# Kernel tuning notes

Hardware: AMD Instinct MI355X
Metric: run time of the kernel (lower is better)

The kernel has to match this reference:

```python
import jax, jax.numpy as jnp
import numpy as np

N = 20000
E = 320000
IN_FEATS = 512
H = 4
D_HID = 256
D_OUT = 256
NEG_SLOPE = 0.2


def _gat_layer(h, src, dst, Wsrc, Wdst, al, ar, b, apply_act):
    # h: [N, Fin]; Wsrc/Wdst: [Fin, H*D]; al/ar: [H, D]; b: [H*D]
    Hh, Dd = al.shape
    fs = (h @ Wsrc).reshape(-1, Hh, Dd)  # [N, H, D] src projection
    fd = (h @ Wdst).reshape(-1, Hh, Dd)  # [N, H, D] dst projection
    el = (fs * al).sum(-1)               # [N, H]
    er = (fd * ar).sum(-1)               # [N, H]
    e = jax.nn.leaky_relu(el[src] + er[dst], NEG_SLOPE)  # [E, H]
    m = jax.lax.stop_gradient(jax.ops.segment_max(e, dst, num_segments=N))
    m = jnp.where(jnp.isfinite(m), m, 0.0)
    ex = jnp.exp(e - m[dst])
    den = jax.ops.segment_sum(ex, dst, num_segments=N)  # [N, H]
    alpha = ex / den[dst]                               # edge softmax per dst node
    msg = fs[src] * alpha[:, :, None]                   # [E, H, D]
    out = jax.ops.segment_sum(msg, dst, num_segments=N) + b.reshape(Hh, Dd)
    if apply_act:
        out = jax.nn.relu(out)
    return out  # [N, H, D]


def setup_inputs() -> dict:
    key = jax.random.key(0)
    ks = jax.random.split(key, 20)
    x = jax.random.normal(ks[0], (N, IN_FEATS), dtype=jnp.float32)
    src = jax.random.randint(ks[1], (E,), 0, N, dtype=jnp.int32)
    dst = jax.random.randint(ks[2], (E,), 0, N, dtype=jnp.int32)
    fins = [IN_FEATS, H * D_HID, H * D_HID]
    douts = [D_HID, D_HID, D_OUT]
    inp = {"x": x, "src": src, "dst": dst}
    ki = 3
    for l in range(3):
        fin, do = fins[l], douts[l]
        s = 1.0 / np.sqrt(fin)
        inp[f"Wsrc{l}"] = jax.random.normal(ks[ki], (fin, H * do), dtype=jnp.float32) * s; ki += 1
        inp[f"Wdst{l}"] = jax.random.normal(ks[ki], (fin, H * do), dtype=jnp.float32) * s; ki += 1
        inp[f"al{l}"] = jax.random.normal(ks[ki], (H, do), dtype=jnp.float32) * 0.1; ki += 1
        inp[f"ar{l}"] = jax.random.normal(ks[ki], (H, do), dtype=jnp.float32) * 0.1; ki += 1
        inp[f"b{l}"] = jnp.zeros((H * do,), dtype=jnp.float32)
    return inp


def reference(x, src, dst,
              Wsrc0, Wdst0, al0, ar0, b0,
              Wsrc1, Wdst1, al1, ar1, b1,
              Wsrc2, Wdst2, al2, ar2, b2):
    h = _gat_layer(x, src, dst, Wsrc0, Wdst0, al0, ar0, b0, True).reshape(N, -1)
    h = _gat_layer(h, src, dst, Wsrc1, Wdst1, al1, ar1, b1, True).reshape(N, -1)
    h = _gat_layer(h, src, dst, Wsrc2, Wdst2, al2, ar2, b2, False)  # [N, H, D_OUT]
    return h.mean(axis=1)  # [N, D_OUT]
```

## Files before the change

kernel.cpp:

```cpp
#include <hip/hip_runtime.h>
#include <hip/hip_bf16.h>
#include <math.h>

#define NNODES 20000
#define NPAD   20480
#define NBM    160
#define NEDGES 320000
#define HEADS  4
#define DDIM   256
#define MCOLS  1024

typedef __attribute__((ext_vector_type(8))) short short8;
typedef __attribute__((ext_vector_type(4))) float f32x4;

__device__ __forceinline__ unsigned short f2bf(float f) {
  unsigned u = __float_as_uint(f);
  unsigned r = (u + 0x7fffu + ((u >> 16) & 1u)) >> 16;
  return (unsigned short)r;
}
__device__ __forceinline__ float bf2f(unsigned short h) {
  return __uint_as_float(((unsigned)h) << 16);
}

__device__ __forceinline__ void async_ld16(void* lds, const void* g) {
  __builtin_amdgcn_global_load_lds(
      (const __attribute__((address_space(1))) unsigned int*)g,
      (__attribute__((address_space(3))) unsigned int*)lds, 16, 0, 0);
}

__global__ void k_zero(int* deg, int n) {
  int i = blockIdx.x*blockDim.x + threadIdx.x;
  if (i < n) deg[i] = 0;
}
__global__ void k_hist(const int* __restrict__ dst, int* deg, int e) {
  int i = blockIdx.x*blockDim.x + threadIdx.x;
  if (i < e) atomicAdd(&deg[dst[i]], 1);
}
__global__ void k_scan(const int* __restrict__ deg, int* row_ptr, int* cursor) {
  __shared__ int sm[1024];
  int t = threadIdx.x;
  const int CH = 20;
  int base = t*CH;
  int s = 0;
  #pragma unroll
  for (int i = 0; i < CH; ++i) { int idx = base+i; if (idx < NNODES) s += deg[idx]; }
  int val = s;
  sm[t] = s; __syncthreads();
  for (int off = 1; off < 1024; off <<= 1) {
    int add = (t >= off) ? sm[t-off] : 0;
    __syncthreads();
    val += add; sm[t] = val;
    __syncthreads();
  }
  int run = val - s;
  for (int i = 0; i < CH; ++i) {
    int idx = base+i;
    if (idx < NNODES) { row_ptr[idx] = run; cursor[idx] = run; run += deg[idx]; }
  }
  if (t == 0) row_ptr[NNODES] = NEDGES;
}
__global__ void k_fill(const int* __restrict__ src, const int* __restrict__ dst,
                       int* cursor, int* srcs_sorted, int* dsts_sorted, int e) {
  int i = blockIdx.x*blockDim.x + threadIdx.x;
  if (i < e) {
    int d = dst[i];
    int pos = atomicAdd(&cursor[d], 1);
    srcs_sorted[pos] = src[i];
    dsts_sorted[pos] = d;
  }
}

__global__ void k_wgt(const float* __restrict__ el, const float* __restrict__ er,
                      const int* __restrict__ srcs, const int* __restrict__ dsts,
                      float* __restrict__ w, int e4) {
  int i = blockIdx.x*blockDim.x + threadIdx.x;
  if (i >= e4) return;
  int pos = i >> 2, h = i & 3;
  float v = el[srcs[pos]*HEADS + h] + er[dsts[pos]*HEADS + h];
  v = v >= 0.f ? v : 0.2f*v;
  w[i] = __expf(v);
}

__global__ void k_fold(const float* __restrict__ W, const float* __restrict__ v,
                       float* __restrict__ F, int K) {
  int wave = threadIdx.x >> 6, lane = threadIdx.x & 63;
  int p = blockIdx.x*4 + wave;
  if (p >= K*HEADS) return;
  int k = p >> 2, h = p & 3;
  const float4 wv = *(const float4*)&W[(size_t)k*MCOLS + h*DDIM + lane*4];
  const float4 av = *(const float4*)&v[h*DDIM + lane*4];
  float s = wv.x*av.x + wv.y*av.y + wv.z*av.z + wv.w*av.w;
  for (int off = 32; off; off >>= 1) s += __shfl_xor(s, off);
  if (lane == 0) F[k*HEADS + h] = s;
}

__global__ void k_cvt_a(const float* __restrict__ x, unsigned short* __restrict__ hi,
                        unsigned short* __restrict__ lo, int total, int total_pad) {
  int i = blockIdx.x*blockDim.x + threadIdx.x;
  int idx = i*4;
  if (idx >= total_pad) return;
  float4 v = (idx < total) ? *(const float4*)&x[idx] : make_float4(0.f,0.f,0.f,0.f);
  ushort4 h, l;
  h.x = f2bf(v.x); l.x = f2bf(v.x - bf2f(h.x));
  h.y = f2bf(v.y); l.y = f2bf(v.y - bf2f(h.y));
  h.z = f2bf(v.z); l.z = f2bf(v.z - bf2f(h.z));
  h.w = f2bf(v.w); l.w = f2bf(v.w - bf2f(h.w));
  *(ushort4*)&hi[idx] = h;
  *(ushort4*)&lo[idx] = l;
}

__global__ __launch_bounds__(256) void k_cvt_w(const float* __restrict__ W,
                                               unsigned short* __restrict__ Th, int K) {
  __shared__ float sm[32][33];
  int k0 = blockIdx.y*32, n0 = blockIdx.x*32;
  int t = threadIdx.x;
  int r = t >> 3, c4 = (t & 7)*4;
  *(float4*)&sm[r][c4] = *(const float4*)&W[(size_t)(k0 + r)*MCOLS + n0 + c4];
  __syncthreads();
  ushort4 h;
  h.x = f2bf(sm[c4+0][r]);
  h.y = f2bf(sm[c4+1][r]);
  h.z = f2bf(sm[c4+2][r]);
  h.w = f2bf(sm[c4+3][r]);
  *(ushort4*)&Th[(size_t)(n0 + r)*K + k0 + c4] = h;
}

__global__ void k_eler0(const float* __restrict__ x, const float* __restrict__ Wal,
                        const float* __restrict__ Wred,
                        float* __restrict__ el, float* __restrict__ er) {
  int n = blockIdx.x;
  int h = threadIdx.x >> 6, lane = threadIdx.x & 63;
  float sl = 0.f, sr = 0.f;
  for (int k = lane; k < 512; k += 64) {
    float xv = x[(size_t)n*512 + k];
    sl = fmaf(xv, Wal[k*HEADS + h], sl);
    sr = fmaf(xv, Wred[k*HEADS + h], sr);
  }
  for (int off = 32; off; off >>= 1) { sl += __shfl_xor(sl, off); sr += __shfl_xor(sr, off); }
  if (lane == 0) { el[n*HEADS + h] = sl; er[n*HEADS + h] = sr; }
}

__global__ __launch_bounds__(256, 3) void k_gemm_mfma(
    const unsigned short* __restrict__ Ah, const unsigned short* __restrict__ Al,
    const unsigned short* __restrict__ Bh,
    unsigned short* __restrict__ Fh, int K) {
  __shared__ short sAh[128*32], sAl[128*32], sBh[128*32];
  const int t = threadIdx.x;
  const int w = t >> 6, l = t & 63;
  const int b = blockIdx.x;
  const int xcd = b & 7, kk = b >> 3;
  const int bm = xcd*20 + (kk >> 3), bn = kk & 7;
  const int m0 = (w >> 1) * 64, n0 = (w & 1) * 64;

  f32x4 acc[4][4];
  #pragma unroll
  for (int i = 0; i < 4; ++i)
    #pragma unroll
    for (int j = 0; j < 4; ++j) acc[i][j] = (f32x4){0.f, 0.f, 0.f, 0.f};

  const int srow = t >> 2, koct = (t & 3) * 8;
  const size_t r64 = (size_t)64 * K;
  const unsigned short* gAh = Ah + (size_t)(bm*128 + srow)*K + koct;
  const unsigned short* gAl = Al + (size_t)(bm*128 + srow)*K + koct;
  const unsigned short* gBh = Bh + (size_t)(bn*128 + srow)*K + koct;
  char* lAh = (char*)sAh + w*1024;
  char* lAl = (char*)sAl + w*1024;
  char* lBh = (char*)sBh + w*1024;

  const int fr = l & 15, fq = l >> 4;

  for (int k0 = 0; k0 < K; k0 += 32) {
    async_ld16(lAh,        gAh + k0);
    async_ld16(lAh + 4096, gAh + k0 + r64);
    async_ld16(lAl,        gAl + k0);
    async_ld16(lAl + 4096, gAl + k0 + r64);
    async_ld16(lBh,        gBh + k0);
    async_ld16(lBh + 4096, gBh + k0 + r64);
    __syncthreads();

    short8 bhv[4];
    #pragma unroll
    for (int nt = 0; nt < 4; ++nt)
      bhv[nt] = *(const short8*)&sBh[(n0 + nt*16 + fr)*32 + fq*8];
    #pragma unroll
    for (int mt = 0; mt < 4; ++mt) {
      int off = (m0 + mt*16 + fr)*32 + fq*8;
      short8 ah = *(const short8*)&sAh[off];
      short8 al = *(const short8*)&sAl[off];
      #pragma unroll
      for (int nt = 0; nt < 4; ++nt) {
        acc[mt][nt] = __builtin_amdgcn_mfma_f32_16x16x32_bf16(ah, bhv[nt], acc[mt][nt], 0, 0, 0);
        acc[mt][nt] = __builtin_amdgcn_mfma_f32_16x16x32_bf16(al, bhv[nt], acc[mt][nt], 0, 0, 0);
      }
    }
    __syncthreads();
  }

  #pragma unroll
  for (int mt = 0; mt < 4; ++mt)
    #pragma unroll
    for (int nt = 0; nt < 4; ++nt) {
      size_t base = (size_t)(bm*128 + m0 + mt*16 + fq*4)*MCOLS + bn*128 + n0 + nt*16 + fr;
      Fh[base          ] = f2bf(acc[mt][nt][0]);
      Fh[base + MCOLS  ] = f2bf(acc[mt][nt][1]);
      Fh[base + 2*MCOLS] = f2bf(acc[mt][nt][2]);
      Fh[base + 3*MCOLS] = f2bf(acc[mt][nt][3]);
    }
}

__global__ __launch_bounds__(256) void k_agg_f(
    const unsigned short* __restrict__ fsh, const float* __restrict__ wbuf,
    const int* __restrict__ row_ptr, const int* __restrict__ srcs,
    const float* __restrict__ bias,
    const float* __restrict__ WalN, const float* __restrict__ WredN,
    unsigned short* __restrict__ Ahi, unsigned short* __restrict__ Alo,
    float* __restrict__ el_next, float* __restrict__ er_next) {
  __shared__ float red_sm[HEADS][8];
  int n = blockIdx.x;
  int h = threadIdx.x >> 6, lane = threadIdx.x & 63;
  int k0 = h*DDIM + lane*4;
  if (n >= NNODES) {
    ushort4 z = {0,0,0,0};
    *(ushort4*)&Ahi[(size_t)n*MCOLS + k0] = z;
    *(ushort4*)&Alo[(size_t)n*MCOLS + k0] = z;
    return;
  }
  int beg = row_ptr[n], end = row_ptr[n+1];
  float den = 0.f;
  float4 acc = make_float4(0.f, 0.f, 0.f, 0.f);
  const char* fbyte = (const char*)fsh;
  const unsigned tb = (unsigned)(k0*2);
  int i = beg;
  for (; i + 3 < end; i += 4) {
    float w0 = wbuf[(size_t)(i  )*HEADS + h];
    float w1 = wbuf[(size_t)(i+1)*HEADS + h];
    float w2 = wbuf[(size_t)(i+2)*HEADS + h];
    float w3 = wbuf[(size_t)(i+3)*HEADS + h];
    unsigned o0 = (unsigned)srcs[i  ]*2048u + tb;
    unsigned o1 = (unsigned)srcs[i+1]*2048u + tb;
    unsigned o2 = (unsigned)srcs[i+2]*2048u + tb;
    unsigned o3 = (unsigned)srcs[i+3]*2048u + tb;
    const ushort4 u0 = *(const ushort4*)(fbyte + o0);
    const ushort4 u1 = *(const ushort4*)(fbyte + o1);
    const ushort4 u2 = *(const ushort4*)(fbyte + o2);
    const ushort4 u3 = *(const ushort4*)(fbyte + o3);
    den += (w0 + w1) + (w2 + w3);
    acc.x = fmaf(w0, bf2f(u0.x), fmaf(w1, bf2f(u1.x), fmaf(w2, bf2f(u2.x), fmaf(w3, bf2f(u3.x), acc.x))));
    acc.y = fmaf(w0, bf2f(u0.y), fmaf(w1, bf2f(u1.y), fmaf(w2, bf2f(u2.y), fmaf(w3, bf2f(u3.y), acc.y))));
    acc.z = fmaf(w0, bf2f(u0.z), fmaf(w1, bf2f(u1.z), fmaf(w2, bf2f(u2.z), fmaf(w3, bf2f(u3.z), acc.z))));
    acc.w = fmaf(w0, bf2f(u0.w), fmaf(w1, bf2f(u1.w), fmaf(w2, bf2f(u2.w), fmaf(w3, bf2f(u3.w), acc.w))));
  }
  for (; i < end; ++i) {
    float wgt = wbuf[(size_t)i*HEADS + h];
    unsigned o = (unsigned)srcs[i]*2048u + tb;
    const ushort4 u = *(const ushort4*)(fbyte + o);
    den += wgt;
    acc.x = fmaf(wgt, bf2f(u.x), acc.x);
    acc.y = fmaf(wgt, bf2f(u.y), acc.y);
    acc.z = fmaf(wgt, bf2f(u.z), acc.z);
    acc.w = fmaf(wgt, bf2f(u.w), acc.w);
  }
  float inv = den > 0.f ? 1.f/den : 0.f;
  const float4 bv = *(const float4*)&bias[k0];
  float4 o;
  o.x = fmaxf(acc.x*inv + bv.x, 0.f);
  o.y = fmaxf(acc.y*inv + bv.y, 0.f);
  o.z = fmaxf(acc.z*inv + bv.z, 0.f);
  o.w = fmaxf(acc.w*inv + bv.w, 0.f);
  ushort4 hv, lv;
  hv.x = f2bf(o.x); lv.x = f2bf(o.x - bf2f(hv.x));
  hv.y = f2bf(o.y); lv.y = f2bf(o.y - bf2f(hv.y));
  hv.z = f2bf(o.z); lv.z = f2bf(o.z - bf2f(hv.z));
  hv.w = f2bf(o.w); lv.w = f2bf(o.w - bf2f(hv.w));
  *(ushort4*)&Ahi[(size_t)n*MCOLS + k0] = hv;
  *(ushort4*)&Alo[(size_t)n*MCOLS + k0] = lv;
  const float4 a0 = *(const float4*)&WalN[(k0+0)*HEADS];
  const float4 a1 = *(const float4*)&WalN[(k0+1)*HEADS];
  const float4 a2 = *(const float4*)&WalN[(k0+2)*HEADS];
  const float4 a3 = *(const float4*)&WalN[(k0+3)*HEADS];
  const float4 q0 = *(const float4*)&WredN[(k0+0)*HEADS];
  const float4 q1 = *(const float4*)&WredN[(k0+1)*HEADS];
  const float4 q2 = *(const float4*)&WredN[(k0+2)*HEADS];
  const float4 q3 = *(const float4*)&WredN[(k0+3)*HEADS];
  float p[8];
  p[0] = o.x*a0.x + o.y*a1.x + o.z*a2.x + o.w*a3.x;
  p[1] = o.x*a0.y + o.y*a1.y + o.z*a2.y + o.w*a3.y;
  p[2] = o.x*a0.z + o.y*a1.z + o.z*a2.z + o.w*a3.z;
  p[3] = o.x*a0.w + o.y*a1.w + o.z*a2.w + o.w*a3.w;
  p[4] = o.x*q0.x + o.y*q1.x + o.z*q2.x + o.w*q3.x;
  p[5] = o.x*q0.y + o.y*q1.y + o.z*q2.y + o.w*q3.y;
  p[6] = o.x*q0.z + o.y*q1.z + o.z*q2.z + o.w*q3.z;
  p[7] = o.x*q0.w + o.y*q1.w + o.z*q2.w + o.w*q3.w;
  for (int off = 32; off; off >>= 1)
    #pragma unroll
    for (int j = 0; j < 8; ++j) p[j] += __shfl_xor(p[j], off);
  if (lane == 0)
    #pragma unroll
    for (int j = 0; j < 8; ++j) red_sm[h][j] = p[j];
  __syncthreads();
  if (threadIdx.x < 8) {
    int t = threadIdx.x;
    float v = (red_sm[0][t] + red_sm[1][t]) + (red_sm[2][t] + red_sm[3][t]);
    if (t < 4) el_next[n*HEADS + t] = v;
    else       er_next[n*HEADS + (t-4)] = v;
  }
}

__global__ __launch_bounds__(256) void k_agg_out(
    const unsigned short* __restrict__ fsh, const float* __restrict__ wbuf,
    const int* __restrict__ row_ptr, const int* __restrict__ srcs,
    const float* __restrict__ bias, float* __restrict__ out) {
  __shared__ float sm[HEADS*DDIM];
  int n = blockIdx.x;
  int h = threadIdx.x >> 6, lane = threadIdx.x & 63;
  int beg = row_ptr[n], end = row_ptr[n+1];
  float den = 0.f;
  float4 acc = make_float4(0.f, 0.f, 0.f, 0.f);
  const char* fbyte = (const char*)fsh;
  const unsigned tb = (unsigned)((h*DDIM + lane*4)*2);
  int i = beg;
  for (; i + 3 < end; i += 4) {
    float w0 = wbuf[(size_t)(i  )*HEADS + h];
    float w1 = wbuf[(size_t)(i+1)*HEADS + h];
    float w2 = wbuf[(size_t)(i+2)*HEADS + h];
    float w3 = wbuf[(size_t)(i+3)*HEADS + h];
    unsigned o0 = (unsigned)srcs[i  ]*2048u + tb;
    unsigned o1 = (unsigned)srcs[i+1]*2048u + tb;
    unsigned o2 = (unsigned)srcs[i+2]*2048u + tb;
    unsigned o3 = (unsigned)srcs[i+3]*2048u + tb;
    const ushort4 u0 = *(const ushort4*)(fbyte + o0);
    const ushort4 u1 = *(const ushort4*)(fbyte + o1);
    const ushort4 u2 = *(const ushort4*)(fbyte + o2);
    const ushort4 u3 = *(const ushort4*)(fbyte + o3);
    den += (w0 + w1) + (w2 + w3);
    acc.x = fmaf(w0, bf2f(u0.x), fmaf(w1, bf2f(u1.x), fmaf(w2, bf2f(u2.x), fmaf(w3, bf2f(u3.x), acc.x))));
    acc.y = fmaf(w0, bf2f(u0.y), fmaf(w1, bf2f(u1.y), fmaf(w2, bf2f(u2.y), fmaf(w3, bf2f(u3.y), acc.y))));
    acc.z = fmaf(w0, bf2f(u0.z), fmaf(w1, bf2f(u1.z), fmaf(w2, bf2f(u2.z), fmaf(w3, bf2f(u3.z), acc.z))));
    acc.w = fmaf(w0, bf2f(u0.w), fmaf(w1, bf2f(u1.w), fmaf(w2, bf2f(u2.w), fmaf(w3, bf2f(u3.w), acc.w))));
  }
  for (; i < end; ++i) {
    float wgt = wbuf[(size_t)i*HEADS + h];
    unsigned o = (unsigned)srcs[i]*2048u + tb;
    const ushort4 u = *(const ushort4*)(fbyte + o);
    den += wgt;
    acc.x = fmaf(wgt, bf2f(u.x), acc.x);
    acc.y = fmaf(wgt, bf2f(u.y), acc.y);
    acc.z = fmaf(wgt, bf2f(u.z), acc.z);
    acc.w = fmaf(wgt, bf2f(u.w), acc.w);
  }
  float inv = den > 0.f ? 1.f/den : 0.f;
  const float4 bv = *(const float4*)&bias[h*DDIM + lane*4];
  acc.x = acc.x*inv + bv.x;
  acc.y = acc.y*inv + bv.y;
  acc.z = acc.z*inv + bv.z;
  acc.w = acc.w*inv + bv.w;
  *(float4*)&sm[h*DDIM + lane*4] = acc;
  __syncthreads();
  int t = threadIdx.x;
  out[(size_t)n*DDIM + t] =
      0.25f*((sm[t] + sm[DDIM + t]) + (sm[2*DDIM + t] + sm[3*DDIM + t]));
}

extern "C" void kernel_launch(void* const* d_in, const int* in_sizes, int n_in,
                              void* d_out, int out_size, void* d_ws, size_t ws_size,
                              hipStream_t stream) {
  const float* x   = (const float*)d_in[0];
  const int*   src = (const int*)d_in[1];
  const int*   dst = (const int*)d_in[2];
  const float* Wsrc[3] = {(const float*)d_in[3], (const float*)d_in[8],  (const float*)d_in[13]};
  const float* Wdst[3] = {(const float*)d_in[4], (const float*)d_in[9],  (const float*)d_in[14]};
  const float* al[3]   = {(const float*)d_in[5], (const float*)d_in[10], (const float*)d_in[15]};
  const float* ar[3]   = {(const float*)d_in[6], (const float*)d_in[11], (const float*)d_in[16]};
  const float* bb[3]   = {(const float*)d_in[7], (const float*)d_in[12], (const float*)d_in[17]};

  char* ws = (char*)d_ws;
  size_t off = 0;
  auto alloc = [&](size_t bytes) { void* p = ws + off; off += (bytes + 255) & ~255ull; return p; };
  unsigned short* fshB = (unsigned short*)alloc((size_t)NPAD*MCOLS*2);
  unsigned short* Ahi = (unsigned short*)alloc((size_t)NPAD*MCOLS*2);
  unsigned short* Alo = (unsigned short*)alloc((size_t)NPAD*MCOLS*2);
  unsigned short* Wth = (unsigned short*)alloc((size_t)MCOLS*MCOLS*2);
  float* elA  = (float*)alloc((size_t)NNODES*HEADS*4);
  float* elB  = (float*)alloc((size_t)NNODES*HEADS*4);
  float* erA  = (float*)alloc((size_t)NNODES*HEADS*4);
  float* erB  = (float*)alloc((size_t)NNODES*HEADS*4);
  float* wbuf = (float*)alloc((size_t)NEDGES*HEADS*4);
  float* WredB[3]; float* WalB[3];
  for (int l = 0; l < 3; ++l) {
    WredB[l] = (float*)alloc(1024*HEADS*4);
    WalB[l]  = (float*)alloc(1024*HEADS*4);
  }
  int* deg     = (int*)alloc((size_t)NNODES*4);
  int* row_ptr = (int*)alloc((size_t)(NNODES+1)*4);
  int* cursor  = (int*)alloc((size_t)NNODES*4);
  int* srcs    = (int*)alloc((size_t)NEDGES*4);
  int* dsts    = (int*)alloc((size_t)NEDGES*4);
  (void)ws_size; (void)in_sizes; (void)n_in; (void)out_size;

  k_zero<<<(NNODES+255)/256, 256, 0, stream>>>(deg, NNODES);
  k_hist<<<(NEDGES+255)/256, 256, 0, stream>>>(dst, deg, NEDGES);
  k_scan<<<1, 1024, 0, stream>>>(deg, row_ptr, cursor);
  k_fill<<<(NEDGES+255)/256, 256, 0, stream>>>(src, dst, cursor, srcs, dsts, NEDGES);

  const int Fin[3] = {512, 1024, 1024};
  for (int l = 0; l < 3; ++l) {
    k_fold<<<Fin[l], 256, 0, stream>>>(Wdst[l], ar[l], WredB[l], Fin[l]);
    k_fold<<<Fin[l], 256, 0, stream>>>(Wsrc[l], al[l], WalB[l], Fin[l]);
  }

  k_cvt_a<<<(NPAD*512/4 + 255)/256, 256, 0, stream>>>(x, Ahi, Alo, NNODES*512, NPAD*512);
  k_eler0<<<NNODES, 256, 0, stream>>>(x, WalB[0], WredB[0], elA, erA);

  float* el_cur = elA; float* el_nxt = elB;
  float* er_cur = erA; float* er_nxt = erB;
  const int E4 = NEDGES*HEADS;
  for (int l = 0; l < 3; ++l) {
    int K = Fin[l];
    dim3 gw(MCOLS/32, K/32);
    k_cvt_w<<<gw, 256, 0, stream>>>(Wsrc[l], Wth, K);
    k_gemm_mfma<<<NBM*8, 256, 0, stream>>>(Ahi, Alo, Wth, fshB, K);
    k_wgt<<<(E4 + 255)/256, 256, 0, stream>>>(el_cur, er_cur, srcs, dsts, wbuf, E4);
    if (l < 2) {
      k_agg_f<<<NPAD, 256, 0, stream>>>(fshB, wbuf, row_ptr, srcs, bb[l],
                                        WalB[l+1], WredB[l+1], Ahi, Alo, el_nxt, er_nxt);
      float* t1 = el_cur; el_cur = el_nxt; el_nxt = t1;
      float* t2 = er_cur; er_cur = er_nxt; er_nxt = t2;
    } else {
      k_agg_out<<<NNODES, 256, 0, stream>>>(fshB, wbuf, row_ptr, srcs, bb[l],
                                            (float*)d_out);
    }
  }
}
```

Measured before the change: 812.3 us.

## Fuse small prep kernels and widen aggregation gathers to 16-byte loads

Merges the six weight-fold launches into one kernel, fuses the layer-0 activation split with the el/er projection, and fuses the per-layer weight transpose/convert with the edge-weight computation, cutting launch count and re-reading of x. The aggregation kernels now use 128 threads per node, with each lane gathering 8 bf16 features through a 16-byte load instead of 4 through an 8-byte load. This halves the number of gather instructions per edge and reduces per-block thread count, at the cost of more registers per lane and less parallelism per node.

```diff
diff --git a/kernel.cpp b/kernel.cpp
--- a/kernel.cpp
+++ b/kernel.cpp
@@ -21,6 +21,8 @@
 __device__ __forceinline__ float bf2f(unsigned short h) {
   return __uint_as_float(((unsigned)h) << 16);
 }
+__device__ __forceinline__ float blo(unsigned v) { return __uint_as_float(v << 16); }
+__device__ __forceinline__ float bhi(unsigned v) { return __uint_as_float(v & 0xffff0000u); }
 
 __device__ __forceinline__ void async_ld16(void* lds, const void* g) {
   __builtin_amdgcn_global_load_lds(
@@ -70,22 +72,11 @@
   }
 }
 
-__global__ void k_wgt(const float* __restrict__ el, const float* __restrict__ er,
-                      const int* __restrict__ srcs, const int* __restrict__ dsts,
-                      float* __restrict__ w, int e4) {
-  int i = blockIdx.x*blockDim.x + threadIdx.x;
-  if (i >= e4) return;
-  int pos = i >> 2, h = i & 3;
-  float v = el[srcs[pos]*HEADS + h] + er[dsts[pos]*HEADS + h];
-  v = v >= 0.f ? v : 0.2f*v;
-  w[i] = __expf(v);
-}
-
-__global__ void k_fold(const float* __restrict__ W, const float* __restrict__ v,
-                       float* __restrict__ F, int K) {
+__device__ __forceinline__ void fold_body(const float* __restrict__ W,
+                                          const float* __restrict__ v,
+                                          float* __restrict__ F, int K, int bb) {
   int wave = threadIdx.x >> 6, lane = threadIdx.x & 63;
-  int p = blockIdx.x*4 + wave;
-  if (p >= K*HEADS) return;
+  int p = bb*4 + wave;
   int k = p >> 2, h = p & 3;
   const float4 wv = *(const float4*)&W[(size_t)k*MCOLS + h*DDIM + lane*4];
   const float4 av = *(const float4*)&v[h*DDIM + lane*4];
@@ -93,51 +84,95 @@
   for (int off = 32; off; off >>= 1) s += __shfl_xor(s, off);
   if (lane == 0) F[k*HEADS + h] = s;
 }
-
-__global__ void k_cvt_a(const float* __restrict__ x, unsigned short* __restrict__ hi,
-                        unsigned short* __restrict__ lo, int total, int total_pad) {
-  int i = blockIdx.x*blockDim.x + threadIdx.x;
-  int idx = i*4;
-  if (idx >= total_pad) return;
-  float4 v = (idx < total) ? *(const float4*)&x[idx] : make_float4(0.f,0.f,0.f,0.f);
-  ushort4 h, l;
-  h.x = f2bf(v.x); l.x = f2bf(v.x - bf2f(h.x));
-  h.y = f2bf(v.y); l.y = f2bf(v.y - bf2f(h.y));
-  h.z = f2bf(v.z); l.z = f2bf(v.z - bf2f(h.z));
-  h.w = f2bf(v.w); l.w = f2bf(v.w - bf2f(h.w));
-  *(ushort4*)&hi[idx] = h;
-  *(ushort4*)&lo[idx] = l;
-}
-
-__global__ __launch_bounds__(256) void k_cvt_w(const float* __restrict__ W,
-                                               unsigned short* __restrict__ Th, int K) {
-  __shared__ float sm[32][33];
-  int k0 = blockIdx.y*32, n0 = blockIdx.x*32;
-  int t = threadIdx.x;
-  int r = t >> 3, c4 = (t & 7)*4;
-  *(float4*)&sm[r][c4] = *(const float4*)&W[(size_t)(k0 + r)*MCOLS + n0 + c4];
+__global__ __launch_bounds__(256) void k_fold_all(
+    const float* Wd0, const float* ar0, float* F0,
+    const float* Ws0, const float* al0, float* G0,
+    const float* Wd1, const float* ar1, float* F1,
+    const float* Ws1, const float* al1, float* G1,
+    const float* Wd2, const float* ar2, float* F2,
+    const float* Ws2, const float* al2, float* G2) {
+  int b = blockIdx.x;
+  if      (b < 512)  fold_body(Wd0, ar0, F0, 512,  b);
+  else if (b < 1024) fold_body(Ws0, al0, G0, 512,  b - 512);
+  else if (b < 2048) fold_body(Wd1, ar1, F1, 1024, b - 1024);
+  else if (b < 3072) fold_body(Ws1, al1, G1, 1024, b - 2048);
+  else if (b < 4096) fold_body(Wd2, ar2, F2, 1024, b - 3072);
+  else               fold_body(Ws2, al2, G2, 1024, b - 4096);
+}
+
+__global__ __launch_bounds__(256) void k_prep0(
+    const float* __restrict__ x, const float* __restrict__ Wal,
+    const float* __restrict__ Wred,
+    unsigned short* __restrict__ hi, unsigned short* __restrict__ lo,
+    float* __restrict__ el, float* __restrict__ er) {
+  __shared__ float red_sm[4][8];
+  int n = blockIdx.x, t = threadIdx.x;
+  if (n >= NNODES) {
+    *(ushort2*)&hi[(size_t)n*512 + 2*t] = (ushort2){0,0};
+    *(ushort2*)&lo[(size_t)n*512 + 2*t] = (ushort2){0,0};
+    return;
+  }
+  float2 xv = *(const float2*)&x[(size_t)n*512 + 2*t];
+  ushort2 h2, l2;
+  h2.x = f2bf(xv.x); l2.x = f2bf(xv.x - bf2f(h2.x));
+  h2.y = f2bf(xv.y); l2.y = f2bf(xv.y - bf2f(h2.y));
+  *(ushort2*)&hi[(size_t)n*512 + 2*t] = h2;
+  *(ushort2*)&lo[(size_t)n*512 + 2*t] = l2;
+  const float4 wa0 = *(const float4*)&Wal[(2*t)*4];
+  const float4 wa1 = *(const float4*)&Wal[(2*t+1)*4];
+  const float4 wr0 = *(const float4*)&Wred[(2*t)*4];
+  const float4 wr1 = *(const float4*)&Wred[(2*t+1)*4];
+  float p[8];
+  p[0] = xv.x*wa0.x + xv.y*wa1.x;
+  p[1] = xv.x*wa0.y + xv.y*wa1.y;
+  p[2] = xv.x*wa0.z + xv.y*wa1.z;
+  p[3] = xv.x*wa0.w + xv.y*wa1.w;
+  p[4] = xv.x*wr0.x + xv.y*wr1.x;
+  p[5] = xv.x*wr0.y + xv.y*wr1.y;
+  p[6] = xv.x*wr0.z + xv.y*wr1.z;
+  p[7] = xv.x*wr0.w + xv.y*wr1.w;
+  for (int off = 32; off; off >>= 1)
+    #pragma unroll
+    for (int j = 0; j < 8; ++j) p[j] += __shfl_xor(p[j], off);
+  if ((t & 63) == 0)
+    #pragma unroll
+    for (int j = 0; j < 8; ++j) red_sm[t >> 6][j] = p[j];
   __syncthreads();
-  ushort4 h;
-  h.x = f2bf(sm[c4+0][r]);
-  h.y = f2bf(sm[c4+1][r]);
-  h.z = f2bf(sm[c4+2][r]);
-  h.w = f2bf(sm[c4+3][r]);
-  *(ushort4*)&Th[(size_t)(n0 + r)*K + k0 + c4] = h;
-}
-
-__global__ void k_eler0(const float* __restrict__ x, const float* __restrict__ Wal,
-                        const float* __restrict__ Wred,
-                        float* __restrict__ el, float* __restrict__ er) {
-  int n = blockIdx.x;
-  int h = threadIdx.x >> 6, lane = threadIdx.x & 63;
-  float sl = 0.f, sr = 0.f;
-  for (int k = lane; k < 512; k += 64) {
-    float xv = x[(size_t)n*512 + k];
-    sl = fmaf(xv, Wal[k*HEADS + h], sl);
-    sr = fmaf(xv, Wred[k*HEADS + h], sr);
-  }
-  for (int off = 32; off; off >>= 1) { sl += __shfl_xor(sl, off); sr += __shfl_xor(sr, off); }
-  if (lane == 0) { el[n*HEADS + h] = sl; er[n*HEADS + h] = sr; }
+  if (t < 8) {
+    float v = (red_sm[0][t] + red_sm[1][t]) + (red_sm[2][t] + red_sm[3][t]);
+    if (t < 4) el[n*HEADS + t] = v;
+    else       er[n*HEADS + (t-4)] = v;
+  }
+}
+
+__global__ __launch_bounds__(256) void k_cvtw_wgt(
+    const float* __restrict__ W, unsigned short* __restrict__ Th, int K,
+    const float* __restrict__ el, const float* __restrict__ er,
+    const int* __restrict__ srcs, const int* __restrict__ dsts,
+    float* __restrict__ wb, int e4) {
+  int b = blockIdx.x;
+  if (b < K) {
+    __shared__ float sm[32][33];
+    int n0 = (b & 31)*32, k0 = (b >> 5)*32;
+    int t = threadIdx.x;
+    int r = t >> 3, c4 = (t & 7)*4;
+    *(float4*)&sm[r][c4] = *(const float4*)&W[(size_t)(k0 + r)*MCOLS + n0 + c4];
+    __syncthreads();
+    ushort4 h;
+    h.x = f2bf(sm[c4+0][r]);
+    h.y = f2bf(sm[c4+1][r]);
+    h.z = f2bf(sm[c4+2][r]);
+    h.w = f2bf(sm[c4+3][r]);
+    *(ushort4*)&Th[(size_t)(n0 + r)*K + k0 + c4] = h;
+  } else {
+    int i = (b - K)*256 + threadIdx.x;
+    if (i < e4) {
+      int pos = i >> 2, h = i & 3;
+      float v = el[srcs[pos]*HEADS + h] + er[dsts[pos]*HEADS + h];
+      v = v >= 0.f ? v : 0.2f*v;
+      wb[i] = __expf(v);
+    }
+  }
 }
 
 __global__ __launch_bounds__(256, 3) void k_gemm_mfma(
@@ -208,157 +243,207 @@
     }
 }
 
-__global__ __launch_bounds__(256) void k_agg_f(
+__global__ __launch_bounds__(128) void k_agg_f(
     const unsigned short* __restrict__ fsh, const float* __restrict__ wbuf,
     const int* __restrict__ row_ptr, const int* __restrict__ srcs,
     const float* __restrict__ bias,
     const float* __restrict__ WalN, const float* __restrict__ WredN,
     unsigned short* __restrict__ Ahi, unsigned short* __restrict__ Alo,
     float* __restrict__ el_next, float* __restrict__ er_next) {
-  __shared__ float red_sm[HEADS][8];
+  __shared__ float red_sm[2][8];
   int n = blockIdx.x;
-  int h = threadIdx.x >> 6, lane = threadIdx.x & 63;
-  int k0 = h*DDIM + lane*4;
+  int t = threadIdx.x;
+  int w = t >> 6, lane = t & 63;
+  int half = lane >> 5, lam = lane & 31;
+  int head = w*2 + half;
+  int k0 = head*DDIM + lam*8;
   if (n >= NNODES) {
-    ushort4 z = {0,0,0,0};
-    *(ushort4*)&Ahi[(size_t)n*MCOLS + k0] = z;
-    *(ushort4*)&Alo[(size_t)n*MCOLS + k0] = z;
+    uint4 z = {0,0,0,0};
+    *(uint4*)&Ahi[(size_t)n*MCOLS + k0] = z;
+    *(uint4*)&Alo[(size_t)n*MCOLS + k0] = z;
     return;
   }
   int beg = row_ptr[n], end = row_ptr[n+1];
   float den = 0.f;
-  float4 acc = make_float4(0.f, 0.f, 0.f, 0.f);
+  float ac[8];
+  #pragma unroll
+  for (int j = 0; j < 8; ++j) ac[j] = 0.f;
   const char* fbyte = (const char*)fsh;
   const unsigned tb = (unsigned)(k0*2);
   int i = beg;
   for (; i + 3 < end; i += 4) {
-    float w0 = wbuf[(size_t)(i  )*HEADS + h];
-    float w1 = wbuf[(size_t)(i+1)*HEADS + h];
-    float w2 = wbuf[(size_t)(i+2)*HEADS + h];
-    float w3 = wbuf[(size_t)(i+3)*HEADS + h];
-    unsigned o0 = (unsigned)srcs[i  ]*2048u + tb;
-    unsigned o1 = (unsigned)srcs[i+1]*2048u + tb;
-    unsigned o2 = (unsigned)srcs[i+2]*2048u + tb;
-    unsigned o3 = (unsigned)srcs[i+3]*2048u + tb;
-    const ushort4 u0 = *(const ushort4*)(fbyte + o0);
-    const ushort4 u1 = *(const ushort4*)(fbyte + o1);
-    const ushort4 u2 = *(const ushort4*)(fbyte + o2);
-    const ushort4 u3 = *(const ushort4*)(fbyte + o3);
+    int s0 = srcs[i], s1 = srcs[i+1], s2 = srcs[i+2], s3 = srcs[i+3];
+    float2 wv0 = *(const float2*)&wbuf[(size_t)(i  )*HEADS + w*2];
+    float2 wv1 = *(const float2*)&wbuf[(size_t)(i+1)*HEADS + w*2];
+    float2 wv2 = *(const float2*)&wbuf[(size_t)(i+2)*HEADS + w*2];
+    float2 wv3 = *(const float2*)&wbuf[(size_t)(i+3)*HEADS + w*2];
+    const uint4 u0 = *(const uint4*)(fbyte + ((unsigned)s0*2048u + tb));
+    const uint4 u1 = *(const uint4*)(fbyte + ((unsigned)s1*2048u + tb));
+    const uint4 u2 = *(const uint4*)(fbyte + ((unsigned)s2*2048u + tb));
+    const uint4 u3 = *(const uint4*)(fbyte + ((unsigned)s3*2048u + tb));
+    float w0 = half ? wv0.y : wv0.x;
+    float w1 = half ? wv1.y : wv1.x;
+    float w2 = half ? wv2.y : wv2.x;
+    float w3 = half ? wv3.y : wv3.x;
     den += (w0 + w1) + (w2 + w3);
-    acc.x = fmaf(w0, bf2f(u0.x), fmaf(w1, bf2f(u1.x), fmaf(w2, bf2f(u2.x), fmaf(w3, bf2f(u3.x), acc.x))));
-    acc.y = fmaf(w0, bf2f(u0.y), fmaf(w1, bf2f(u1.y), fmaf(w2, bf2f(u2.y), fmaf(w3, bf2f(u3.y), acc.y))));
-    acc.z = fmaf(w0, bf2f(u0.z), fmaf(w1, bf2f(u1.z), fmaf(w2, bf2f(u2.z), fmaf(w3, bf2f(u3.z), acc.z))));
-    acc.w = fmaf(w0, bf2f(u0.w), fmaf(w1, bf2f(u1.w), fmaf(w2, bf2f(u2.w), fmaf(w3, bf2f(u3.w), acc.w))));
+    ac[0] = fmaf(w0, blo(u0.x), fmaf(w1, blo(u1.x), fmaf(w2, blo(u2.x), fmaf(w3, blo(u3.x), ac[0]))));
+    ac[1] = fmaf(w0, bhi(u0.x), fmaf(w1, bhi(u1.x), fmaf(w2, bhi(u2.x), fmaf(w3, bhi(u3.x), ac[1]))));
+    ac[2] = fmaf(w0, blo(u0.y), fmaf(w1, blo(u1.y), fmaf(w2, blo(u2.y), fmaf(w3, blo(u3.y), ac[2]))));
+    ac[3] = fmaf(w0, bhi(u0.y), fmaf(w1, bhi(u1.y), fmaf(w2, bhi(u2.y), fmaf(w3, bhi(u3.y), ac[3]))));
+    ac[4] = fmaf(w0, blo(u0.z), fmaf(w1, blo(u1.z), fmaf(w2, blo(u2.z), fmaf(w3, blo(u3.z), ac[4]))));
+    ac[5] = fmaf(w0, bhi(u0.z), fmaf(w1, bhi(u1.z), fmaf(w2, bhi(u2.z), fmaf(w3, bhi(u3.z), ac[5]))));
+    ac[6] = fmaf(w0, blo(u0.w), fmaf(w1, blo(u1.w), fmaf(w2, blo(u2.w), fmaf(w3, blo(u3.w), ac[6]))));
+    ac[7] = fmaf(w0, bhi(u0.w), fmaf(w1, bhi(u1.w), fmaf(w2, bhi(u2.w), fmaf(w3, bhi(u3.w), ac[7]))));
   }
   for (; i < end; ++i) {
-    float wgt = wbuf[(size_t)i*HEADS + h];
-    unsigned o = (unsigned)srcs[i]*2048u + tb;
-    const ushort4 u = *(const ushort4*)(fbyte + o);
+    int s = srcs[i];
+    float2 wv = *(const float2*)&wbuf[(size_t)i*HEADS + w*2];
+    float wgt = half ? wv.y : wv.x;
+    const uint4 u = *(const uint4*)(fbyte + ((unsigned)s*2048u + tb));
     den += wgt;
-    acc.x = fmaf(wgt, bf2f(u.x), acc.x);
-    acc.y = fmaf(wgt, bf2f(u.y), acc.y);
-    acc.z = fmaf(wgt, bf2f(u.z), acc.z);
-    acc.w = fmaf(wgt, bf2f(u.w), acc.w);
+    ac[0] = fmaf(wgt, blo(u.x), ac[0]);
+    ac[1] = fmaf(wgt, bhi(u.x), ac[1]);
+    ac[2] = fmaf(wgt, blo(u.y), ac[2]);
+    ac[3] = fmaf(wgt, bhi(u.y), ac[3]);
+    ac[4] = fmaf(wgt, blo(u.z), ac[4]);
+    ac[5] = fmaf(wgt, bhi(u.z), ac[5]);
+    ac[6] = fmaf(wgt, blo(u.w), ac[6]);
+    ac[7] = fmaf(wgt, bhi(u.w), ac[7]);
   }
   float inv = den > 0.f ? 1.f/den : 0.f;
-  const float4 bv = *(const float4*)&bias[k0];
-  float4 o;
-  o.x = fmaxf(acc.x*inv + bv.x, 0.f);
-  o.y = fmaxf(acc.y*inv + bv.y, 0.f);
-  o.z = fmaxf(acc.z*inv + bv.z, 0.f);
-  o.w = fmaxf(acc.w*inv + bv.w, 0.f);
-  ushort4 hv, lv;
-  hv.x = f2bf(o.x); lv.x = f2bf(o.x - bf2f(hv.x));
-  hv.y = f2bf(o.y); lv.y = f2bf(o.y - bf2f(hv.y));
-  hv.z = f2bf(o.z); lv.z = f2bf(o.z - bf2f(hv.z));
-  hv.w = f2bf(o.w); lv.w = f2bf(o.w - bf2f(hv.w));
-  *(ushort4*)&Ahi[(size_t)n*MCOLS + k0] = hv;
-  *(ushort4*)&Alo[(size_t)n*MCOLS + k0] = lv;
-  const float4 a0 = *(const float4*)&WalN[(k0+0)*HEADS];
-  const float4 a1 = *(const float4*)&WalN[(k0+1)*HEADS];
-  const float4 a2 = *(const float4*)&WalN[(k0+2)*HEADS];
-  const float4 a3 = *(const float4*)&WalN[(k0+3)*HEADS];
-  const float4 q0 = *(const float4*)&WredN[(k0+0)*HEADS];
-  const float4 q1 = *(const float4*)&WredN[(k0+1)*HEADS];
-  const float4 q2 = *(const float4*)&WredN[(k0+2)*HEADS];
-  const float4 q3 = *(const float4*)&WredN[(k0+3)*HEADS];
+  const float4 bv0 = *(const float4*)&bias[k0];
+  const float4 bv1 = *(const float4*)&bias[k0 + 4];
+  float o[8];
+  o[0] = fmaxf(ac[0]*inv + bv0.x, 0.f);
+  o[1] = fmaxf(ac[1]*inv + bv0.y, 0.f);
+  o[2] = fmaxf(ac[2]*inv + bv0.z, 0.f);
+  o[3] = fmaxf(ac[3]*inv + bv0.w, 0.f);
+  o[4] = fmaxf(ac[4]*inv + bv1.x, 0.f);
+  o[5] = fmaxf(ac[5]*inv + bv1.y, 0.f);
+  o[6] = fmaxf(ac[6]*inv + bv1.z, 0.f);
+  o[7] = fmaxf(ac[7]*inv + bv1.w, 0.f);
+  uint4 hp, lp;
+  unsigned h0, h1;
+  h0 = f2bf(o[0]); h1 = f2bf(o[1]); hp.x = h0 | (h1 << 16);
+  lp.x = (unsigned)f2bf(o[0] - bf2f((unsigned short)h0)) |
+         ((unsigned)f2bf(o[1] - bf2f((unsigned short)h1)) << 16);
+  h0 = f2bf(o[2]); h1 = f2bf(o[3]); hp.y = h0 | (h1 << 16);
+  lp.y = (unsigned)f2bf(o[2] - bf2f((unsigned short)h0)) |
+         ((unsigned)f2bf(o[3] - bf2f((unsigned short)h1)) << 16);
+  h0 = f2bf(o[4]); h1 = f2bf(o[5]); hp.z = h0 | (h1 << 16);
+  lp.z = (unsigned)f2bf(o[4] - bf2f((unsigned short)h0)) |
+         ((unsigned)f2bf(o[5] - bf2f((unsigned short)h1)) << 16);
+  h0 = f2bf(o[6]); h1 = f2bf(o[7]); hp.w = h0 | (h1 << 16);
+  lp.w = (unsigned)f2bf(o[6] - bf2f((unsigned short)h0)) |
+         ((unsigned)f2bf(o[7] - bf2f((unsigned short)h1)) << 16);
+  *(uint4*)&Ahi[(size_t)n*MCOLS + k0] = hp;
+  *(uint4*)&Alo[(size_t)n*MCOLS + k0] = lp;
   float p[8];
-  p[0] = o.x*a0.x + o.y*a1.x + o.z*a2.x + o.w*a3.x;
-  p[1] = o.x*a0.y + o.y*a1.y + o.z*a2.y + o.w*a3.y;
-  p[2] = o.x*a0.z + o.y*a1.z + o.z*a2.z + o.w*a3.z;
-  p[3] = o.x*a0.w + o.y*a1.w + o.z*a2.w + o.w*a3.w;
-  p[4] = o.x*q0.x + o.y*q1.x + o.z*q2.x + o.w*q3.x;
-  p[5] = o.x*q0.y + o.y*q1.y + o.z*q2.y + o.w*q3.y;
-  p[6] = o.x*q0.z + o.y*q1.z + o.z*q2.z + o.w*q3.z;
-  p[7] = o.x*q0.w + o.y*q1.w + o.z*q2.w + o.w*q3.w;
+  #pragma unroll
+  for (int j = 0; j < 8; ++j) p[j] = 0.f;
+  #pragma unroll
+  for (int j = 0; j < 8; ++j) {
+    const float4 wa = *(const float4*)&WalN[(k0+j)*HEADS];
+    const float4 wr = *(const float4*)&WredN[(k0+j)*HEADS];
+    p[0] = fmaf(o[j], wa.x, p[0]);
+    p[1] = fmaf(o[j], wa.y, p[1]);
+    p[2] = fmaf(o[j], wa.z, p[2]);
+    p[3] = fmaf(o[j], wa.w, p[3]);
+    p[4] = fmaf(o[j], wr.x, p[4]);
+    p[5] = fmaf(o[j], wr.y, p[5]);
+    p[6] = fmaf(o[j], wr.z, p[6]);
+    p[7] = fmaf(o[j], wr.w, p[7]);
+  }
   for (int off = 32; off; off >>= 1)
     #pragma unroll
     for (int j = 0; j < 8; ++j) p[j] += __shfl_xor(p[j], off);
   if (lane == 0)
     #pragma unroll
-    for (int j = 0; j < 8; ++j) red_sm[h][j] = p[j];
+    for (int j = 0; j < 8; ++j) red_sm[w][j] = p[j];
   __syncthreads();
-  if (threadIdx.x < 8) {
-    int t = threadIdx.x;
-    float v = (red_sm[0][t] + red_sm[1][t]) + (red_sm[2][t] + red_sm[3][t]);
+  if (t < 8) {
+    float v = red_sm[0][t] + red_sm[1][t];
     if (t < 4) el_next[n*HEADS + t] = v;
     else       er_next[n*HEADS + (t-4)] = v;
   }
 }
 
-__global__ __launch_bounds__(256) void k_agg_out(
+__global__ __launch_bounds__(128) void k_agg_out(
     const unsigned short* __restrict__ fsh, const float* __restrict__ wbuf,
     const int* __restrict__ row_ptr, const int* __restrict__ srcs,
     const float* __restrict__ bias, float* __restrict__ out) {
   __shared__ float sm[HEADS*DDIM];
   int n = blockIdx.x;
-  int h = threadIdx.x >> 6, lane = threadIdx.x & 63;
+  int t = threadIdx.x;
+  int w = t >> 6, lane = t & 63;
+  int half = lane >> 5, lam = lane & 31;
+  int head = w*2 + half;
+  int k0 = head*DDIM + lam*8;
   int beg = row_ptr[n], end = row_ptr[n+1];
   float den = 0.f;
-  float4 acc = make_float4(0.f, 0.f, 0.f, 0.f);
+  float ac[8];
+  #pragma unroll
+  for (int j = 0; j < 8; ++j) ac[j] = 0.f;
   const char* fbyte = (const char*)fsh;
-  const unsigned tb = (unsigned)((h*DDIM + lane*4)*2);
+  const unsigned tb = (unsigned)(k0*2);
   int i = beg;
   for (; i + 3 < end; i += 4) {
-    float w0 = wbuf[(size_t)(i  )*HEADS + h];
-    float w1 = wbuf[(size_t)(i+1)*HEADS + h];
-    float w2 = wbuf[(size_t)(i+2)*HEADS + h];
-    float w3 = wbuf[(size_t)(i+3)*HEADS + h];
-    unsigned o0 = (unsigned)srcs[i  ]*2048u + tb;
-    unsigned o1 = (unsigned)srcs[i+1]*2048u + tb;
-    unsigned o2 = (unsigned)srcs[i+2]*2048u + tb;
-    unsigned o3 = (unsigned)srcs[i+3]*2048u + tb;
-    const ushort4 u0 = *(const ushort4*)(fbyte + o0);
-    const ushort4 u1 = *(const ushort4*)(fbyte + o1);
-    const ushort4 u2 = *(const ushort4*)(fbyte + o2);
-    const ushort4 u3 = *(const ushort4*)(fbyte + o3);
+    int s0 = srcs[i], s1 = srcs[i+1], s2 = srcs[i+2], s3 = srcs[i+3];
+    float2 wv0 = *(const float2*)&wbuf[(size_t)(i  )*HEADS + w*2];
+    float2 wv1 = *(const float2*)&wbuf[(size_t)(i+1)*HEADS + w*2];
+    float2 wv2 = *(const float2*)&wbuf[(size_t)(i+2)*HEADS + w*2];
+    float2 wv3 = *(const float2*)&wbuf[(size_t)(i+3)*HEADS + w*2];
+    const uint4 u0 = *(const uint4*)(fbyte + ((unsigned)s0*2048u + tb));
+    const uint4 u1 = *(const uint4*)(fbyte + ((unsigned)s1*2048u + tb));
+    const uint4 u2 = *(const uint4*)(fbyte + ((unsigned)s2*2048u + tb));
+    const uint4 u3 = *(const uint4*)(fbyte + ((unsigned)s3*2048u + tb));
+    float w0 = half ? wv0.y : wv0.x;
+    float w1 = half ? wv1.y : wv1.x;
+    float w2 = half ? wv2.y : wv2.x;
+    float w3 = half ? wv3.y : wv3.x;
     den += (w0 + w1) + (w2 + w3);
-    acc.x = fmaf(w0, bf2f(u0.x), fmaf(w1, bf2f(u1.x), fmaf(w2, bf2f(u2.x), fmaf(w3, bf2f(u3.x), acc.x))));
-    acc.y = fmaf(w0, bf2f(u0.y), fmaf(w1, bf2f(u1.y), fmaf(w2, bf2f(u2.y), fmaf(w3, bf2f(u3.y), acc.y))));
-    acc.z = fmaf(w0, bf2f(u0.z), fmaf(w1, bf2f(u1.z), fmaf(w2, bf2f(u2.z), fmaf(w3, bf2f(u3.z), acc.z))));
-    acc.w = fmaf(w0, bf2f(u0.w), fmaf(w1, bf2f(u1.w), fmaf(w2, bf2f(u2.w), fmaf(w3, bf2f(u3.w), acc.w))));
+    ac[0] = fmaf(w0, blo(u0.x), fmaf(w1, blo(u1.x), fmaf(w2, blo(u2.x), fmaf(w3, blo(u3.x), ac[0]))));
+    ac[1] = fmaf(w0, bhi(u0.x), fmaf(w1, bhi(u1.x), fmaf(w2, bhi(u2.x), fmaf(w3, bhi(u3.x), ac[1]))));
+    ac[2] = fmaf(w0, blo(u0.y), fmaf(w1, blo(u1.y), fmaf(w2, blo(u2.y), fmaf(w3, blo(u3.y), ac[2]))));
+    ac[3] = fmaf(w0, bhi(u0.y), fmaf(w1, bhi(u1.y), fmaf(w2, bhi(u2.y), fmaf(w3, bhi(u3.y), ac[3]))));
+    ac[4] = fmaf(w0, blo(u0.z), fmaf(w1, blo(u1.z), fmaf(w2, blo(u2.z), fmaf(w3, blo(u3.z), ac[4]))));
+    ac[5] = fmaf(w0, bhi(u0.z), fmaf(w1, bhi(u1.z), fmaf(w2, bhi(u2.z), fmaf(w3, bhi(u3.z), ac[5]))));
+    ac[6] = fmaf(w0, blo(u0.w), fmaf(w1, blo(u1.w), fmaf(w2, blo(u2.w), fmaf(w3, blo(u3.w), ac[6]))));
+    ac[7] = fmaf(w0, bhi(u0.w), fmaf(w1, bhi(u1.w), fmaf(w2, bhi(u2.w), fmaf(w3, bhi(u3.w), ac[7]))));
   }
   for (; i < end; ++i) {
-    float wgt = wbuf[(size_t)i*HEADS + h];
-    unsigned o = (unsigned)srcs[i]*2048u + tb;
-    const ushort4 u = *(const ushort4*)(fbyte + o);
+    int s = srcs[i];
+    float2 wv = *(const float2*)&wbuf[(size_t)i*HEADS + w*2];
+    float wgt = half ? wv.y : wv.x;
+    const uint4 u = *(const uint4*)(fbyte + ((unsigned)s*2048u + tb));
     den += wgt;
-    acc.x = fmaf(wgt, bf2f(u.x), acc.x);
-    acc.y = fmaf(wgt, bf2f(u.y), acc.y);
-    acc.z = fmaf(wgt, bf2f(u.z), acc.z);
-    acc.w = fmaf(wgt, bf2f(u.w), acc.w);
+    ac[0] = fmaf(wgt, blo(u.x), ac[0]);
+    ac[1] = fmaf(wgt, bhi(u.x), ac[1]);
+    ac[2] = fmaf(wgt, blo(u.y), ac[2]);
+    ac[3] = fmaf(wgt, bhi(u.y), ac[3]);
+    ac[4] = fmaf(wgt, blo(u.z), ac[4]);
+    ac[5] = fmaf(wgt, bhi(u.z), ac[5]);
+    ac[6] = fmaf(wgt, blo(u.w), ac[6]);
+    ac[7] = fmaf(wgt, bhi(u.w), ac[7]);
   }
   float inv = den > 0.f ? 1.f/den : 0.f;
-  const float4 bv = *(const float4*)&bias[h*DDIM + lane*4];
-  acc.x = acc.x*inv + bv.x;
-  acc.y = acc.y*inv + bv.y;
-  acc.z = acc.z*inv + bv.z;
-  acc.w = acc.w*inv + bv.w;
-  *(float4*)&sm[h*DDIM + lane*4] = acc;
+  const float4 bv0 = *(const float4*)&bias[k0];
+  const float4 bv1 = *(const float4*)&bias[k0 + 4];
+  sm[k0+0] = ac[0]*inv + bv0.x;
+  sm[k0+1] = ac[1]*inv + bv0.y;
+  sm[k0+2] = ac[2]*inv + bv0.z;
+  sm[k0+3] = ac[3]*inv + bv0.w;
+  sm[k0+4] = ac[4]*inv + bv1.x;
+  sm[k0+5] = ac[5]*inv + bv1.y;
+  sm[k0+6] = ac[6]*inv + bv1.z;
+  sm[k0+7] = ac[7]*inv + bv1.w;
   __syncthreads();
-  int t = threadIdx.x;
-  out[(size_t)n*DDIM + t] =
-      0.25f*((sm[t] + sm[DDIM + t]) + (sm[2*DDIM + t] + sm[3*DDIM + t]));
+  #pragma unroll
+  for (int rep = 0; rep < 2; ++rep) {
+    int d = t + rep*128;
+    out[(size_t)n*DDIM + d] =
+        0.25f*((sm[d] + sm[DDIM + d]) + (sm[2*DDIM + d] + sm[3*DDIM + d]));
+  }
 }
 
 extern "C" void kernel_launch(void* const* d_in, const int* in_sizes, int n_in,
@@ -402,31 +487,29 @@
   k_scan<<<1, 1024, 0, stream>>>(deg, row_ptr, cursor);
   k_fill<<<(NEDGES+255)/256, 256, 0, stream>>>(src, dst, cursor, srcs, dsts, NEDGES);
 
-  const int Fin[3] = {512, 1024, 1024};
-  for (int l = 0; l < 3; ++l) {
-    k_fold<<<Fin[l], 256, 0, stream>>>(Wdst[l], ar[l], WredB[l], Fin[l]);
-    k_fold<<<Fin[l], 256, 0, stream>>>(Wsrc[l], al[l], WalB[l], Fin[l]);
-  }
-
-  k_cvt_a<<<(NPAD*512/4 + 255)/256, 256, 0, stream>>>(x, Ahi, Alo, NNODES*512, NPAD*512);
-  k_eler0<<<NNODES, 256, 0, stream>>>(x, WalB[0], WredB[0], elA, erA);
+  k_fold_all<<<5120, 256, 0, stream>>>(
+      Wdst[0], ar[0], WredB[0], Wsrc[0], al[0], WalB[0],
+      Wdst[1], ar[1], WredB[1], Wsrc[1], al[1], WalB[1],
+      Wdst[2], ar[2], WredB[2], Wsrc[2], al[2], WalB[2]);
+
+  k_prep0<<<NPAD, 256, 0, stream>>>(x, WalB[0], WredB[0], Ahi, Alo, elA, erA);
 
   float* el_cur = elA; float* el_nxt = elB;
   float* er_cur = erA; float* er_nxt = erB;
+  const int Fin[3] = {512, 1024, 1024};
   const int E4 = NEDGES*HEADS;
   for (int l = 0; l < 3; ++l) {
     int K = Fin[l];
-    dim3 gw(MCOLS/32, K/32);
-    k_cvt_w<<<gw, 256, 0, stream>>>(Wsrc[l], Wth, K);
+    k_cvtw_wgt<<<K + (E4 + 255)/256, 256, 0, stream>>>(
+        Wsrc[l], Wth, K, el_cur, er_cur, srcs, dsts, wbuf, E4);
     k_gemm_mfma<<<NBM*8, 256, 0, stream>>>(Ahi, Alo, Wth, fshB, K);
-    k_wgt<<<(E4 + 255)/256, 256, 0, stream>>>(el_cur, er_cur, srcs, dsts, wbuf, E4);
     if (l < 2) {
-      k_agg_f<<<NPAD, 256, 0, stream>>>(fshB, wbuf, row_ptr, srcs, bb[l],
+      k_agg_f<<<NPAD, 128, 0, stream>>>(fshB, wbuf, row_ptr, srcs, bb[l],
                                         WalB[l+1], WredB[l+1], Ahi, Alo, el_nxt, er_nxt);
       float* t1 = el_cur; el_cur = el_nxt; el_nxt = t1;
       float* t2 = er_cur; er_cur = er_nxt; er_nxt = t2;
     } else {
-      k_agg_out<<<NNODES, 256, 0, stream>>>(fshB, wbuf, row_ptr, srcs, bb[l],
+      k_agg_out<<<NNODES, 128, 0, stream>>>(fshB, wbuf, row_ptr, srcs, bb[l],
                                             (float*)d_out);
     }
   }
```

New measurement: 804.1 us. Within noise of the previous version (-1.0%).
